# Performance work log

Measured on AMD Instinct MI355X. Metric: run time of the kernel, lower is better.

The kernel has to match this reference:

```python
import jax, jax.numpy as jnp
import numpy as np

N_X, DIS, IN, OUT = 40000, 10000, 128, 64
N = N_X + DIS
E = 800000
BN_EPS = 1e-5


def setup_inputs() -> dict:
    key = jax.random.key(0)
    ks = jax.random.split(key, 20)

    def glorot(k, shape):
        fan_in, fan_out = shape[-2], shape[-1]
        a = np.sqrt(6.0 / (fan_in + fan_out)).astype(np.float32)
        return jax.random.uniform(k, shape, jnp.float32, -a, a)

    return {
        "x": jax.random.normal(ks[0], (N_X, IN), jnp.float32),
        "emb": jax.random.uniform(ks[1], (DIS, IN), jnp.float32),
        "conv1_w": glorot(ks[2], (3, IN, 2 * OUT)),
        "conv1_root": glorot(ks[3], (IN, 2 * OUT)),
        "conv1_bias": jnp.zeros((2 * OUT,), jnp.float32),
        "conv2_w": glorot(ks[4], (3, 2 * OUT, 4 * OUT)),
        "conv2_root": glorot(ks[5], (2 * OUT, 4 * OUT)),
        "conv2_bias": jnp.zeros((4 * OUT,), jnp.float32),
        "convinf_w": glorot(ks[6], (3, 4 * OUT, 4 * OUT)),
        "convinf_root": glorot(ks[7], (4 * OUT, 4 * OUT)),
        "convinf_bias": jnp.zeros((4 * OUT,), jnp.float32),
        "conv3_w": glorot(ks[8], (3, 4 * OUT, OUT)),
        "conv3_root": glorot(ks[9], (4 * OUT, OUT)),
        "conv3_bias": jnp.zeros((OUT,), jnp.float32),
        "norm1_g": jnp.ones((2 * OUT,), jnp.float32),
        "norm1_b": jnp.zeros((2 * OUT,), jnp.float32),
        "norm2_g": jnp.ones((4 * OUT,), jnp.float32),
        "norm2_b": jnp.zeros((4 * OUT,), jnp.float32),
        "edge_index": jax.random.randint(ks[10], (2, E), 0, N),
        "edge_types": jax.random.randint(ks[11], (E,), 0, 3),
    }


def reference(x, emb, conv1_w, conv1_root, conv1_bias, conv2_w, conv2_root,
              conv2_bias, convinf_w, convinf_root, convinf_bias, conv3_w,
              conv3_root, conv3_bias, norm1_g, norm1_b, norm2_g, norm2_b,
              edge_index, edge_types):
    dst, src = edge_index[0], edge_index[1]  # adj_t row = target, col = source
    n = x.shape[0] + emb.shape[0]

    # gcn_norm without self-loops: deg over rows, w_e = d^-1/2[dst] * d^-1/2[src]
    deg = jax.ops.segment_sum(jnp.ones(dst.shape[0], jnp.float32), dst, num_segments=n)
    dis = jnp.where(deg > 0, jax.lax.rsqrt(jnp.maximum(deg, 1.0)), 0.0)
    ew = dis[dst] * dis[src]  # [E]

    def wrgcn(h, W, root, bias):
        out = h @ root + bias
        h_src = h[src]  # [E, d] gather (dominant memory traffic)
        for r in range(3):
            w_r = jnp.where(edge_types == r, ew, 0.0)
            agg = jax.ops.segment_sum(w_r[:, None] * h_src, dst, num_segments=n)
            out = out + agg @ W[r]
        return out

    def bn(h, g, b):
        m = h.mean(axis=0)
        v = jnp.var(h, axis=0)  # biased, matches torch BN training normalization
        return (h - m) * jax.lax.rsqrt(v + BN_EPS) * g + b

    h0 = jnp.concatenate([x, emb], axis=0)  # [N, IN]
    x1 = bn(wrgcn(h0, conv1_w, conv1_root, conv1_bias), norm1_g, norm1_b)
    x2 = bn(wrgcn(jax.nn.relu(x1), conv2_w, conv2_root, conv2_bias), norm2_g, norm2_b)
    for _ in range(5):
        x2 = bn(wrgcn(jax.nn.relu(x2), convinf_w, convinf_root, convinf_bias), norm2_g, norm2_b)
    return wrgcn(jax.nn.relu(x2), conv3_w, conv3_root, conv3_bias)
```

## Files before the change

### kernel.cpp

```cpp
#include <hip/hip_runtime.h>

#define N_X  40000
#define NN   50000
#define NE   800000
#define MPAD 50048

using short8  = __attribute__((ext_vector_type(8))) short;
using floatx4 = __attribute__((ext_vector_type(4))) float;
using uintx2  = __attribute__((ext_vector_type(2))) unsigned int;
using uintx4  = __attribute__((ext_vector_type(4))) unsigned int;

typedef const __attribute__((address_space(1))) void gv_t;
typedef __attribute__((address_space(3))) void lv_t;

__device__ __forceinline__ unsigned short f2bf(float f) {
  unsigned u = __float_as_uint(f);
  u += 0x7FFF + ((u >> 16) & 1);
  return (unsigned short)(u >> 16);
}
__device__ __forceinline__ float bf2f(unsigned v) {
  return __uint_as_float(v << 16);
}
__device__ __forceinline__ float h2f(unsigned v) {
  unsigned short s = (unsigned short)v;
  _Float16 f;
  __builtin_memcpy(&f, &s, 2);
  return (float)f;
}
__device__ __forceinline__ unsigned short f2h(float f) {
  _Float16 h = (_Float16)f;
  unsigned short s;
  __builtin_memcpy(&s, &h, 2);
  return s;
}

__global__ void k_deg(const int* __restrict__ dst, int* __restrict__ deg) {
  int e = blockIdx.x * blockDim.x + threadIdx.x;
  if (e < NE) atomicAdd(&deg[dst[e]], 1);
}

__global__ void k_dis(const int* __restrict__ deg, float* __restrict__ dis) {
  int i = blockIdx.x * blockDim.x + threadIdx.x;
  if (i < NN) dis[i] = deg[i] > 0 ? rsqrtf((float)deg[i]) : 0.f;
}

#define SCAN_B 1024
#define SCAN_NB 49
__global__ void k_scan1(const int* __restrict__ deg, int* __restrict__ rowp,
                        int* __restrict__ bsum) {
  __shared__ int buf[SCAN_B];
  int b = blockIdx.x;
  int i = b * SCAN_B + threadIdx.x;
  int v = (i < NN) ? deg[i] : 0;
  buf[threadIdx.x] = v;
  __syncthreads();
  for (int off = 1; off < SCAN_B; off <<= 1) {
    int t = (threadIdx.x >= off) ? buf[threadIdx.x - off] : 0;
    __syncthreads();
    buf[threadIdx.x] += t;
    __syncthreads();
  }
  if (i < NN) rowp[i] = buf[threadIdx.x] - v;
  if (threadIdx.x == SCAN_B - 1) bsum[b] = buf[SCAN_B - 1];
}

__global__ void k_scan2(int* __restrict__ bsum) {
  if (threadIdx.x == 0) {
    int acc = 0;
    for (int i = 0; i < SCAN_NB; ++i) { int t = bsum[i]; bsum[i] = acc; acc += t; }
  }
}

__global__ void k_scan3(int* __restrict__ rowp, const int* __restrict__ bsum) {
  int i = blockIdx.x * blockDim.x + threadIdx.x;
  if (i < NN) rowp[i] += bsum[i >> 10];
  if (i == 0) rowp[NN] = NE;
}

__global__ void k_build(const int* __restrict__ dst, const int* __restrict__ src,
                        const int* __restrict__ typ, const float* __restrict__ dis,
                        const int* __restrict__ rowp, int* __restrict__ cur,
                        uintx2* __restrict__ ed) {
  int e = blockIdx.x * blockDim.x + threadIdx.x;
  if (e >= NE) return;
  int d = dst[e], s = src[e];
  int p = rowp[d] + atomicAdd(&cur[d], 1);
  uintx2 v;
  v.x = (unsigned)s | ((unsigned)typ[e] << 28);
  v.y = __float_as_uint(dis[d] * dis[s]);
  ed[p] = v;
}

__global__ void k_prep0(const float* __restrict__ x, const float* __restrict__ emb,
                        unsigned short* __restrict__ Gh, unsigned short* __restrict__ Gl) {
  int idx = blockIdx.x * blockDim.x + threadIdx.x;
  if (idx >= NN * 32) return;
  int r = idx >> 5;
  const float* srcp = (r < N_X) ? (x + (size_t)idx * 4)
                                : (emb + ((size_t)idx - (size_t)N_X * 32) * 4);
  float4 hv = *(const float4*)srcp;
  float vv[4] = {hv.x, hv.y, hv.z, hv.w};
  unsigned hw[2], lw[2];
#pragma unroll
  for (int q = 0; q < 2; ++q) {
    unsigned short h0 = f2bf(vv[2 * q]), h1 = f2bf(vv[2 * q + 1]);
    unsigned short l0 = f2bf(vv[2 * q] - bf2f(h0)), l1 = f2bf(vv[2 * q + 1] - bf2f(h1));
    hw[q] = (unsigned)h0 | ((unsigned)h1 << 16);
    lw[q] = (unsigned)l0 | ((unsigned)l1 << 16);
  }
  size_t o = (size_t)idx * 4;
  *(uintx2*)(Gh + o) = uintx2{hw[0], hw[1]};
  *(uintx2*)(Gl + o) = uintx2{lw[0], lw[1]};
}

__global__ void k_prep(const float* __restrict__ H, const float* __restrict__ sc,
                       const float* __restrict__ sh, unsigned short* __restrict__ Gh,
                       unsigned short* __restrict__ Gl, int din) {
  int idx = blockIdx.x * blockDim.x + threadIdx.x;
  if (idx >= NN * (din >> 2)) return;
  int c4 = (idx & ((din >> 2) - 1)) * 4;
  float4 hv = *(const float4*)(H + (size_t)idx * 4);
  float vv[4] = {hv.x, hv.y, hv.z, hv.w};
#pragma unroll
  for (int q = 0; q < 4; ++q)
    vv[q] = fmaxf(vv[q] * sc[c4 + q] + sh[c4 + q], 0.f);
  unsigned hw[2], lw[2];
#pragma unroll
  for (int q = 0; q < 2; ++q) {
    unsigned short h0 = f2bf(vv[2 * q]), h1 = f2bf(vv[2 * q + 1]);
    unsigned short l0 = f2bf(vv[2 * q] - bf2f(h0)), l1 = f2bf(vv[2 * q + 1] - bf2f(h1));
    hw[q] = (unsigned)h0 | ((unsigned)h1 << 16);
    lw[q] = (unsigned)l0 | ((unsigned)l1 << 16);
  }
  size_t o = (size_t)idx * 4;
  *(uintx2*)(Gh + o) = uintx2{hw[0], hw[1]};
  *(uintx2*)(Gl + o) = uintx2{lw[0], lw[1]};
}

__global__ void k_wcat2(const float* __restrict__ root, const float* __restrict__ W,
                        unsigned short* __restrict__ BhT, unsigned short* __restrict__ BlT,
                        int din, int dout) {
  int idx = blockIdx.x * blockDim.x + threadIdx.x;
  if (idx >= 4 * dout * din) return;
  int n = idx / din, k = idx % din;
  float v;
  if (n < dout) v = root[(size_t)k * dout + n];
  else {
    int r = n / dout - 1, c = n % dout;
    v = W[((size_t)r * din + k) * dout + c];
  }
  unsigned short h = f2bf(v);
  BhT[idx] = h;
  BlT[idx] = f2bf(v - bf2f(h));
}

__global__ __launch_bounds__(256, 3) void k_gemm2(
    const unsigned short* __restrict__ Ah, const unsigned short* __restrict__ Al,
    const unsigned short* __restrict__ Bh, const unsigned short* __restrict__ Bl,
    float* __restrict__ Rroot, unsigned short* __restrict__ P,
    int M, int K, int dout, int ny) {
  constexpr int TC = 24;
  constexpr int CPW = 6;
  constexpr int NT = 2;
  __shared__ __align__(16) char lds[2][TC * 1024];

  const int tid = threadIdx.x;
  const int lane = tid & 63;
  const int w = tid >> 6;
  const int wm = w >> 1, wn = w & 1;
  const int r16 = lane & 15, kg = lane >> 4;

  const int nwg = gridDim.x;
  const int q = nwg >> 3, r = nwg & 7;
  const int xcd = blockIdx.x & 7, pos = blockIdx.x >> 3;
  const int t = (xcd < r ? xcd * (q + 1) : r * (q + 1) + (xcd - r) * q) + pos;
  const int bm = (t / ny) * 128;
  const int bn = (t % ny) * 64;

  const int rowseg = lane >> 2;
  const int seg = (lane & 3) ^ ((lane >> 3) & 3);
  const unsigned short* gb[CPW];
#pragma unroll
  for (int i = 0; i < CPW; ++i) {
    int c = w * CPW + i;
    const unsigned short* base;
    int row0;
    if (c < 16) { base = (c < 8) ? Ah : Al; row0 = bm + (c & 7) * 16; }
    else        { int cc = c - 16; base = (cc < 4) ? Bh : Bl; row0 = bn + (cc & 3) * 16; }
    gb[i] = base + (size_t)(row0 + rowseg) * K + seg * 8;
  }

  floatx4 acc[4][NT];
#pragma unroll
  for (int i = 0; i < 4; ++i)
#pragma unroll
    for (int jj = 0; jj < NT; ++jj) acc[i][jj] = (floatx4)0.f;

  const int nk = K >> 5;

  auto stage = [&](int b, int tk) {
#pragma unroll
    for (int i = 0; i < CPW; ++i)
      __builtin_amdgcn_global_load_lds((gv_t*)(gb[i] + tk * 32),
                                       (lv_t*)&lds[b][(w * CPW + i) * 1024],
                                       16, 0, 0);
  };

  stage(0, 0);
  stage(1, 1);

  const int fo = r16 * 64 + ((kg ^ ((r16 >> 1) & 3)) * 16);

  int buf = 0;
  for (int tk = 0; tk < nk; ++tk) {
    if (tk < nk - 1) asm volatile("s_waitcnt vmcnt(6)" ::: "memory");
    else             asm volatile("s_waitcnt vmcnt(0)" ::: "memory");
    __builtin_amdgcn_s_barrier();

    const char* Lb = lds[buf];
    short8 ah[4], al[4], bh[NT], bl[NT];
#pragma unroll
    for (int mt = 0; mt < 4; ++mt) {
      ah[mt] = *(const short8*)(Lb + (wm * 4 + mt) * 1024 + fo);
      al[mt] = *(const short8*)(Lb + (8 + wm * 4 + mt) * 1024 + fo);
    }
#pragma unroll
    for (int nt = 0; nt < NT; ++nt) {
      bh[nt] = *(const short8*)(Lb + (16 + wn * NT + nt) * 1024 + fo);
      bl[nt] = *(const short8*)(Lb + (20 + wn * NT + nt) * 1024 + fo);
    }

    __builtin_amdgcn_s_setprio(1);
#pragma unroll
    for (int mt = 0; mt < 4; ++mt)
#pragma unroll
      for (int nt = 0; nt < NT; ++nt) {
        acc[mt][nt] = __builtin_amdgcn_mfma_f32_16x16x32_bf16(ah[mt], bh[nt], acc[mt][nt], 0, 0, 0);
        acc[mt][nt] = __builtin_amdgcn_mfma_f32_16x16x32_bf16(ah[mt], bl[nt], acc[mt][nt], 0, 0, 0);
        acc[mt][nt] = __builtin_amdgcn_mfma_f32_16x16x32_bf16(al[mt], bh[nt], acc[mt][nt], 0, 0, 0);
      }
    __builtin_amdgcn_s_setprio(0);

    __builtin_amdgcn_s_barrier();
    if (tk + 2 < nk) stage(buf, tk + 2);
    buf ^= 1;
  }

  const int sec = bn / dout;
  const int cb = bn - sec * dout;
#pragma unroll
  for (int mt = 0; mt < 4; ++mt) {
    const int gr0 = bm + wm * 64 + mt * 16 + kg * 4;
#pragma unroll
    for (int nt = 0; nt < NT; ++nt) {
      const int colL = cb + wn * 32 + nt * 16 + r16;
#pragma unroll
      for (int rr = 0; rr < 4; ++rr) {
        const int gr = gr0 + rr;
        if (gr >= M) continue;
        const float o = acc[mt][nt][rr];
        if (sec == 0) Rroot[(size_t)gr * dout + colL] = o;
        else          P[((size_t)gr * 3 + (sec - 1)) * dout + colL] = f2h(o);
      }
    }
  }
}

template <int L>
__global__ void k_agg2(const unsigned short* __restrict__ P,
                       const float* __restrict__ Rroot,
                       const float* __restrict__ bias,
                       const int* __restrict__ rowp, const uintx2* __restrict__ ed,
                       float* __restrict__ Out, int dout) {
  constexpr int G = 64 / L;
  const int wid = (blockIdx.x * 256 + threadIdx.x) >> 6;
  if (wid >= NN) return;
  const int lane = threadIdx.x & 63;
  const int grp = lane / L;
  const int c0 = (lane & (L - 1)) * 4;
  const int beg = rowp[wid], end = rowp[wid + 1];
  float a[4] = {};
  for (int i = beg + grp; i < end; i += G) {
    const uintx2 e = ed[i];
    const float wv = __uint_as_float(e.y);
    const unsigned tt = e.x >> 28;
    const size_t off = ((size_t)(e.x & 0x0FFFFFFFu) * 3 + tt) * dout + c0;
    const uintx2 g = *(const uintx2*)(P + off);
    a[0] += wv * h2f(g.x & 0xFFFFu);
    a[1] += wv * h2f(g.x >> 16);
    a[2] += wv * h2f(g.y & 0xFFFFu);
    a[3] += wv * h2f(g.y >> 16);
  }
  if constexpr (G > 1) {
#pragma unroll
    for (int off = L; off < 64; off <<= 1) {
#pragma unroll
      for (int qq = 0; qq < 4; ++qq) a[qq] += __shfl_xor(a[qq], off);
    }
  }
  if (grp == 0) {
    const float4 bv = *(const float4*)(bias + c0);
    const float4 rv = *(const float4*)(Rroot + (size_t)wid * dout + c0);
    float4 o;
    o.x = rv.x + bv.x + a[0];
    o.y = rv.y + bv.y + a[1];
    o.z = rv.z + bv.z + a[2];
    o.w = rv.w + bv.w + a[3];
    *(float4*)(Out + (size_t)wid * dout + c0) = o;
  }
}

__global__ void k_bnstats(const float* __restrict__ H, float* __restrict__ sums, int d) {
  int c = threadIdx.x;
  float s = 0.f, s2 = 0.f;
  for (int r = blockIdx.x; r < NN; r += gridDim.x) {
    float v = H[(size_t)r * d + c];
    s += v;
    s2 += v * v;
  }
  atomicAdd(&sums[c], s);
  atomicAdd(&sums[d + c], s2);
}

__global__ void k_bnfinal(const float* __restrict__ sums, const float* __restrict__ g,
                          const float* __restrict__ b, float* __restrict__ sc,
                          float* __restrict__ sh, int d) {
  int c = threadIdx.x;
  if (c >= d) return;
  float mean = sums[c] * (1.f / NN);
  float var = sums[d + c] * (1.f / NN) - mean * mean;
  float rs = rsqrtf(var + 1e-5f);
  float s = rs * g[c];
  sc[c] = s;
  sh[c] = b[c] - mean * s;
}

extern "C" void kernel_launch(void* const* d_in, const int* in_sizes, int n_in,
                              void* d_out, int out_size, void* d_ws, size_t ws_size,
                              hipStream_t stream) {
  const float* x   = (const float*)d_in[0];
  const float* emb = (const float*)d_in[1];
  const float* conv_w[4] = {(const float*)d_in[2], (const float*)d_in[5],
                            (const float*)d_in[8], (const float*)d_in[11]};
  const float* conv_r[4] = {(const float*)d_in[3], (const float*)d_in[6],
                            (const float*)d_in[9], (const float*)d_in[12]};
  const float* conv_b[4] = {(const float*)d_in[4], (const float*)d_in[7],
                            (const float*)d_in[10], (const float*)d_in[13]};
  const float* n1g = (const float*)d_in[14];
  const float* n1b = (const float*)d_in[15];
  const float* n2g = (const float*)d_in[16];
  const float* n2b = (const float*)d_in[17];
  const int* eidx = (const int*)d_in[18];
  const int* etyp = (const int*)d_in[19];
  const int* dst  = eidx;
  const int* srcp = eidx + NE;
  float* out = (float*)d_out;

  char* w = (char*)d_ws;
  auto alloc = [&](size_t bytes) {
    char* p = w;
    w += (bytes + 255) & ~(size_t)255;
    return p;
  };
  unsigned short* Gh   = (unsigned short*)alloc((size_t)MPAD * 256 * 2);
  unsigned short* Gl   = (unsigned short*)alloc((size_t)MPAD * 256 * 2);
  unsigned short* P    = (unsigned short*)alloc((size_t)MPAD * 768 * 2);
  float*    Rroot = (float*)alloc((size_t)MPAD * 256 * 4);
  float*    H    = (float*)alloc((size_t)NN * 256 * 4);
  unsigned short* WcTh = (unsigned short*)alloc((size_t)1024 * 256 * 2);
  unsigned short* WcTl = (unsigned short*)alloc((size_t)1024 * 256 * 2);
  float*    bns  = (float*)alloc(512 * 4);
  float*    bsc  = (float*)alloc(256 * 4);
  float*    bsh  = (float*)alloc(256 * 4);
  float*    dis  = (float*)alloc((size_t)NN * 4);
  int*      deg  = (int*)alloc((size_t)NN * 4);
  int*      rowp = (int*)alloc((size_t)(NN + 1) * 4);
  int*      cur  = (int*)alloc((size_t)NN * 4);
  int*      bsum = (int*)alloc(64 * 4);
  uintx2*   ed   = (uintx2*)alloc((size_t)NE * 8);

  hipMemsetAsync(deg, 0, (size_t)NN * 4, stream);
  hipMemsetAsync(cur, 0, (size_t)NN * 4, stream);
  k_deg<<<(NE + 255) / 256, 256, 0, stream>>>(dst, deg);
  k_dis<<<(NN + 255) / 256, 256, 0, stream>>>(deg, dis);
  k_scan1<<<SCAN_NB, SCAN_B, 0, stream>>>(deg, rowp, bsum);
  k_scan2<<<1, 64, 0, stream>>>(bsum);
  k_scan3<<<(NN + 255) / 256, 256, 0, stream>>>(rowp, bsum);
  k_build<<<(NE + 255) / 256, 256, 0, stream>>>(dst, srcp, etyp, dis, rowp, cur, ed);

  const int din_a[8]  = {128, 128, 256, 256, 256, 256, 256, 256};
  const int dout_a[8] = {128, 256, 256, 256, 256, 256, 256, 64};
  const int wi_a[8]   = {0, 1, 2, 2, 2, 2, 2, 3};
  const int gm = (NN + 127) / 128;

  for (int l = 0; l < 8; ++l) {
    const int din = din_a[l], dout = dout_a[l];
    const int wi = wi_a[l];

    if (l == 0)
      k_prep0<<<(NN * 32 + 255) / 256, 256, 0, stream>>>(x, emb, Gh, Gl);
    else
      k_prep<<<(NN * (din >> 2) + 255) / 256, 256, 0, stream>>>(H, bsc, bsh, Gh, Gl, din);

    k_wcat2<<<(4 * dout * din + 255) / 256, 256, 0, stream>>>(conv_r[wi], conv_w[wi],
                                                              WcTh, WcTl, din, dout);

    const int ny = 4 * dout / 64;
    k_gemm2<<<gm * ny, 256, 0, stream>>>(Gh, Gl, WcTh, WcTl, Rroot, P, NN, din, dout, ny);

    float* O = (l == 7) ? out : H;
    if (dout == 256)
      k_agg2<64><<<(NN + 3) / 4, 256, 0, stream>>>(P, Rroot, conv_b[wi], rowp, ed, O, dout);
    else if (dout == 128)
      k_agg2<32><<<(NN + 3) / 4, 256, 0, stream>>>(P, Rroot, conv_b[wi], rowp, ed, O, dout);
    else
      k_agg2<16><<<(NN + 3) / 4, 256, 0, stream>>>(P, Rroot, conv_b[wi], rowp, ed, O, dout);

    if (l < 7) {
      hipMemsetAsync(bns, 0, (size_t)2 * dout * 4, stream);
      k_bnstats<<<256, dout, 0, stream>>>(H, bns, dout);
      k_bnfinal<<<1, 256, 0, stream>>>(bns, (l == 0) ? n1g : n2g,
                                       (l == 0) ? n1b : n2b, bsc, bsh, dout);
    }
  }
}
```

Before: 1.859 ms.

## Fuse BN statistics into aggregation and enlarge GEMM M-tile to 256

The aggregation kernel becomes a grid-stride persistent kernel that accumulates per-column sum and sum-of-squares and flushes them with atomics into 64 slots. This removes the separate BN stats pass that reread H. The GEMM tile grows from 128 to 256 rows with more LDS and lower occupancy, so each B tile is reused across more rows. The larger tile reads padded rows beyond MPAD, which land inside the workspace, and fewer blocks may reduce latency hiding.

```diff
diff --git a/kernel.cpp b/kernel.cpp
--- a/kernel.cpp
+++ b/kernel.cpp
@@ -4,6 +4,7 @@
 #define NN   50000
 #define NE   800000
 #define MPAD 50048
+#define NSLOT 64
 
 using short8  = __attribute__((ext_vector_type(8))) short;
 using floatx4 = __attribute__((ext_vector_type(4))) float;
@@ -154,13 +155,13 @@
   BlT[idx] = f2bf(v - bf2f(h));
 }
 
-__global__ __launch_bounds__(256, 3) void k_gemm2(
+__global__ __launch_bounds__(256, 2) void k_gemm2(
     const unsigned short* __restrict__ Ah, const unsigned short* __restrict__ Al,
     const unsigned short* __restrict__ Bh, const unsigned short* __restrict__ Bl,
     float* __restrict__ Rroot, unsigned short* __restrict__ P,
     int M, int K, int dout, int ny) {
-  constexpr int TC = 24;
-  constexpr int CPW = 6;
+  constexpr int TC = 40;
+  constexpr int CPW = 10;
   constexpr int NT = 2;
   __shared__ __align__(16) char lds[2][TC * 1024];
 
@@ -174,7 +175,7 @@
   const int q = nwg >> 3, r = nwg & 7;
   const int xcd = blockIdx.x & 7, pos = blockIdx.x >> 3;
   const int t = (xcd < r ? xcd * (q + 1) : r * (q + 1) + (xcd - r) * q) + pos;
-  const int bm = (t / ny) * 128;
+  const int bm = (t / ny) * 256;
   const int bn = (t % ny) * 64;
 
   const int rowseg = lane >> 2;
@@ -185,14 +186,16 @@
     int c = w * CPW + i;
     const unsigned short* base;
     int row0;
-    if (c < 16) { base = (c < 8) ? Ah : Al; row0 = bm + (c & 7) * 16; }
-    else        { int cc = c - 16; base = (cc < 4) ? Bh : Bl; row0 = bn + (cc & 3) * 16; }
+    if (c < 16)      { base = Ah; row0 = bm + c * 16; }
+    else if (c < 32) { base = Al; row0 = bm + (c - 16) * 16; }
+    else if (c < 36) { base = Bh; row0 = bn + (c - 32) * 16; }
+    else             { base = Bl; row0 = bn + (c - 36) * 16; }
     gb[i] = base + (size_t)(row0 + rowseg) * K + seg * 8;
   }
 
-  floatx4 acc[4][NT];
-#pragma unroll
-  for (int i = 0; i < 4; ++i)
+  floatx4 acc[8][NT];
+#pragma unroll
+  for (int i = 0; i < 8; ++i)
 #pragma unroll
     for (int jj = 0; jj < NT; ++jj) acc[i][jj] = (floatx4)0.f;
 
@@ -213,32 +216,30 @@
 
   int buf = 0;
   for (int tk = 0; tk < nk; ++tk) {
-    if (tk < nk - 1) asm volatile("s_waitcnt vmcnt(6)" ::: "memory");
+    if (tk < nk - 1) asm volatile("s_waitcnt vmcnt(10)" ::: "memory");
     else             asm volatile("s_waitcnt vmcnt(0)" ::: "memory");
     __builtin_amdgcn_s_barrier();
 
     const char* Lb = lds[buf];
-    short8 ah[4], al[4], bh[NT], bl[NT];
-#pragma unroll
-    for (int mt = 0; mt < 4; ++mt) {
-      ah[mt] = *(const short8*)(Lb + (wm * 4 + mt) * 1024 + fo);
-      al[mt] = *(const short8*)(Lb + (8 + wm * 4 + mt) * 1024 + fo);
-    }
+    short8 bh[NT], bl[NT];
 #pragma unroll
     for (int nt = 0; nt < NT; ++nt) {
-      bh[nt] = *(const short8*)(Lb + (16 + wn * NT + nt) * 1024 + fo);
-      bl[nt] = *(const short8*)(Lb + (20 + wn * NT + nt) * 1024 + fo);
+      bh[nt] = *(const short8*)(Lb + (32 + wn * NT + nt) * 1024 + fo);
+      bl[nt] = *(const short8*)(Lb + (36 + wn * NT + nt) * 1024 + fo);
     }
 
     __builtin_amdgcn_s_setprio(1);
 #pragma unroll
-    for (int mt = 0; mt < 4; ++mt)
+    for (int mt = 0; mt < 8; ++mt) {
+      short8 ah = *(const short8*)(Lb + (wm * 8 + mt) * 1024 + fo);
+      short8 al = *(const short8*)(Lb + (16 + wm * 8 + mt) * 1024 + fo);
 #pragma unroll
       for (int nt = 0; nt < NT; ++nt) {
-        acc[mt][nt] = __builtin_amdgcn_mfma_f32_16x16x32_bf16(ah[mt], bh[nt], acc[mt][nt], 0, 0, 0);
-        acc[mt][nt] = __builtin_amdgcn_mfma_f32_16x16x32_bf16(ah[mt], bl[nt], acc[mt][nt], 0, 0, 0);
-        acc[mt][nt] = __builtin_amdgcn_mfma_f32_16x16x32_bf16(al[mt], bh[nt], acc[mt][nt], 0, 0, 0);
+        acc[mt][nt] = __builtin_amdgcn_mfma_f32_16x16x32_bf16(ah, bh[nt], acc[mt][nt], 0, 0, 0);
+        acc[mt][nt] = __builtin_amdgcn_mfma_f32_16x16x32_bf16(ah, bl[nt], acc[mt][nt], 0, 0, 0);
+        acc[mt][nt] = __builtin_amdgcn_mfma_f32_16x16x32_bf16(al, bh[nt], acc[mt][nt], 0, 0, 0);
       }
+    }
     __builtin_amdgcn_s_setprio(0);
 
     __builtin_amdgcn_s_barrier();
@@ -249,8 +250,8 @@
   const int sec = bn / dout;
   const int cb = bn - sec * dout;
 #pragma unroll
-  for (int mt = 0; mt < 4; ++mt) {
-    const int gr0 = bm + wm * 64 + mt * 16 + kg * 4;
+  for (int mt = 0; mt < 8; ++mt) {
+    const int gr0 = bm + wm * 128 + mt * 16 + kg * 4;
 #pragma unroll
     for (int nt = 0; nt < NT; ++nt) {
       const int colL = cb + wn * 32 + nt * 16 + r16;
@@ -271,68 +272,78 @@
                        const float* __restrict__ Rroot,
                        const float* __restrict__ bias,
                        const int* __restrict__ rowp, const uintx2* __restrict__ ed,
-                       float* __restrict__ Out, int dout) {
+                       float* __restrict__ Out, float* __restrict__ bns, int dout) {
   constexpr int G = 64 / L;
-  const int wid = (blockIdx.x * 256 + threadIdx.x) >> 6;
-  if (wid >= NN) return;
   const int lane = threadIdx.x & 63;
   const int grp = lane / L;
   const int c0 = (lane & (L - 1)) * 4;
-  const int beg = rowp[wid], end = rowp[wid + 1];
-  float a[4] = {};
-  for (int i = beg + grp; i < end; i += G) {
-    const uintx2 e = ed[i];
-    const float wv = __uint_as_float(e.y);
-    const unsigned tt = e.x >> 28;
-    const size_t off = ((size_t)(e.x & 0x0FFFFFFFu) * 3 + tt) * dout + c0;
-    const uintx2 g = *(const uintx2*)(P + off);
-    a[0] += wv * h2f(g.x & 0xFFFFu);
-    a[1] += wv * h2f(g.x >> 16);
-    a[2] += wv * h2f(g.y & 0xFFFFu);
-    a[3] += wv * h2f(g.y >> 16);
-  }
-  if constexpr (G > 1) {
-#pragma unroll
-    for (int off = L; off < 64; off <<= 1) {
-#pragma unroll
-      for (int qq = 0; qq < 4; ++qq) a[qq] += __shfl_xor(a[qq], off);
-    }
-  }
-  if (grp == 0) {
-    const float4 bv = *(const float4*)(bias + c0);
-    const float4 rv = *(const float4*)(Rroot + (size_t)wid * dout + c0);
-    float4 o;
-    o.x = rv.x + bv.x + a[0];
-    o.y = rv.y + bv.y + a[1];
-    o.z = rv.z + bv.z + a[2];
-    o.w = rv.w + bv.w + a[3];
-    *(float4*)(Out + (size_t)wid * dout + c0) = o;
-  }
-}
-
-__global__ void k_bnstats(const float* __restrict__ H, float* __restrict__ sums, int d) {
-  int c = threadIdx.x;
-  float s = 0.f, s2 = 0.f;
-  for (int r = blockIdx.x; r < NN; r += gridDim.x) {
-    float v = H[(size_t)r * d + c];
-    s += v;
-    s2 += v * v;
-  }
-  atomicAdd(&sums[c], s);
-  atomicAdd(&sums[d + c], s2);
-}
-
-__global__ void k_bnfinal(const float* __restrict__ sums, const float* __restrict__ g,
+  const int wid0 = (blockIdx.x * 256 + threadIdx.x) >> 6;
+  const int nw = gridDim.x * 4;
+
+  float bs[4] = {}, bs2[4] = {};
+  float4 bv;
+  if (grp == 0) bv = *(const float4*)(bias + c0);
+
+  for (int wid = wid0; wid < NN; wid += nw) {
+    const int beg = rowp[wid], end = rowp[wid + 1];
+    float a[4] = {};
+    for (int i = beg + grp; i < end; i += G) {
+      const uintx2 e = ed[i];
+      const float wv = __uint_as_float(e.y);
+      const unsigned tt = e.x >> 28;
+      const size_t off = ((size_t)(e.x & 0x0FFFFFFFu) * 3 + tt) * dout + c0;
+      const uintx2 g = *(const uintx2*)(P + off);
+      a[0] += wv * h2f(g.x & 0xFFFFu);
+      a[1] += wv * h2f(g.x >> 16);
+      a[2] += wv * h2f(g.y & 0xFFFFu);
+      a[3] += wv * h2f(g.y >> 16);
+    }
+    if constexpr (G > 1) {
+#pragma unroll
+      for (int off = L; off < 64; off <<= 1) {
+#pragma unroll
+        for (int qq = 0; qq < 4; ++qq) a[qq] += __shfl_xor(a[qq], off);
+      }
+    }
+    if (grp == 0) {
+      const float4 rv = *(const float4*)(Rroot + (size_t)wid * dout + c0);
+      float o[4];
+      o[0] = rv.x + bv.x + a[0];
+      o[1] = rv.y + bv.y + a[1];
+      o[2] = rv.z + bv.z + a[2];
+      o[3] = rv.w + bv.w + a[3];
+      *(float4*)(Out + (size_t)wid * dout + c0) =
+          make_float4(o[0], o[1], o[2], o[3]);
+#pragma unroll
+      for (int qq = 0; qq < 4; ++qq) { bs[qq] += o[qq]; bs2[qq] += o[qq] * o[qq]; }
+    }
+  }
+  if (bns && grp == 0) {
+    float* sl = bns + (size_t)(blockIdx.x & (NSLOT - 1)) * 1024;
+#pragma unroll
+    for (int qq = 0; qq < 4; ++qq) {
+      atomicAdd(&sl[c0 + qq], bs[qq]);
+      atomicAdd(&sl[512 + c0 + qq], bs2[qq]);
+    }
+  }
+}
+
+__global__ void k_bnfinal(const float* __restrict__ bns, const float* __restrict__ g,
                           const float* __restrict__ b, float* __restrict__ sc,
                           float* __restrict__ sh, int d) {
   int c = threadIdx.x;
   if (c >= d) return;
-  float mean = sums[c] * (1.f / NN);
-  float var = sums[d + c] * (1.f / NN) - mean * mean;
+  float s = 0.f, s2 = 0.f;
+  for (int i = 0; i < NSLOT; ++i) {
+    s += bns[(size_t)i * 1024 + c];
+    s2 += bns[(size_t)i * 1024 + 512 + c];
+  }
+  float mean = s * (1.f / NN);
+  float var = s2 * (1.f / NN) - mean * mean;
   float rs = rsqrtf(var + 1e-5f);
-  float s = rs * g[c];
-  sc[c] = s;
-  sh[c] = b[c] - mean * s;
+  float scale = rs * g[c];
+  sc[c] = scale;
+  sh[c] = b[c] - mean * scale;
 }
 
 extern "C" void kernel_launch(void* const* d_in, const int* in_sizes, int n_in,
@@ -369,7 +380,7 @@
   float*    H    = (float*)alloc((size_t)NN * 256 * 4);
   unsigned short* WcTh = (unsigned short*)alloc((size_t)1024 * 256 * 2);
   unsigned short* WcTl = (unsigned short*)alloc((size_t)1024 * 256 * 2);
-  float*    bns  = (float*)alloc(512 * 4);
+  float*    bns  = (float*)alloc((size_t)NSLOT * 1024 * 4);
   float*    bsc  = (float*)alloc(256 * 4);
   float*    bsh  = (float*)alloc(256 * 4);
   float*    dis  = (float*)alloc((size_t)NN * 4);
@@ -391,7 +402,7 @@
   const int din_a[8]  = {128, 128, 256, 256, 256, 256, 256, 256};
   const int dout_a[8] = {128, 256, 256, 256, 256, 256, 256, 64};
   const int wi_a[8]   = {0, 1, 2, 2, 2, 2, 2, 3};
-  const int gm = (NN + 127) / 128;
+  const int gm = (MPAD + 255) / 256;
 
   for (int l = 0; l < 8; ++l) {
     const int din = din_a[l], dout = dout_a[l];
@@ -408,19 +419,19 @@
     const int ny = 4 * dout / 64;
     k_gemm2<<<gm * ny, 256, 0, stream>>>(Gh, Gl, WcTh, WcTl, Rroot, P, NN, din, dout, ny);
 
+    if (l < 7) hipMemsetAsync(bns, 0, (size_t)NSLOT * 1024 * 4, stream);
+
     float* O = (l == 7) ? out : H;
+    float* bstat = (l == 7) ? nullptr : bns;
     if (dout == 256)
-      k_agg2<64><<<(NN + 3) / 4, 256, 0, stream>>>(P, Rroot, conv_b[wi], rowp, ed, O, dout);
+      k_agg2<64><<<2048, 256, 0, stream>>>(P, Rroot, conv_b[wi], rowp, ed, O, bstat, dout);
     else if (dout == 128)
-      k_agg2<32><<<(NN + 3) / 4, 256, 0, stream>>>(P, Rroot, conv_b[wi], rowp, ed, O, dout);
+      k_agg2<32><<<2048, 256, 0, stream>>>(P, Rroot, conv_b[wi], rowp, ed, O, bstat, dout);
     else
-      k_agg2<16><<<(NN + 3) / 4, 256, 0, stream>>>(P, Rroot, conv_b[wi], rowp, ed, O, dout);
-
-    if (l < 7) {
-      hipMemsetAsync(bns, 0, (size_t)2 * dout * 4, stream);
-      k_bnstats<<<256, dout, 0, stream>>>(H, bns, dout);
+      k_agg2<16><<<2048, 256, 0, stream>>>(P, Rroot, conv_b[wi], rowp, ed, O, bstat, dout);
+
+    if (l < 7)
       k_bnfinal<<<1, 256, 0, stream>>>(bns, (l == 0) ? n1g : n2g,
                                        (l == 0) ? n1b : n2b, bsc, bsh, dout);
-    }
-  }
-}
+  }
+}
```

After: 2.085 ms. +12.2%, slower.
